# Performance work log

Hardware: AMD Instinct MI355X
Metric: run time of the kernel (lower is better)

The kernel has to match this reference:

```python
import jax, jax.numpy as jnp
import numpy as np

N_P, N_A, N_S = 100000, 150000, 1000
D_IN, N_HID, N_OUT = 256, 256, 64
E_PA, E_PS = 800000, 100000
HOP = 3


def spmm(row, col, val, h, n_rows):
    # sparse A (edge list) @ dense h : gather source rows, scale, scatter-add to dest rows
    return jax.ops.segment_sum(val[:, None] * h[col], row, num_segments=n_rows)


def setup_inputs() -> dict:
    key = jax.random.key(0)
    ks = jax.random.split(key, 30)
    inp = {}
    inp['x_P'] = jax.random.normal(ks[0], (N_P, D_IN), jnp.float32)
    inp['x_A'] = jax.random.normal(ks[1], (N_A, D_IN), jnp.float32)
    inp['x_S'] = jax.random.normal(ks[2], (N_S, D_IN), jnp.float32)
    inp['pa_row'] = jax.random.randint(ks[3], (E_PA,), 0, N_P, jnp.int32)
    inp['pa_col'] = jax.random.randint(ks[4], (E_PA,), 0, N_A, jnp.int32)
    inp['pa_val'] = jax.random.uniform(ks[5], (E_PA,), jnp.float32)
    inp['ps_row'] = jax.random.randint(ks[6], (E_PS,), 0, N_P, jnp.int32)
    inp['ps_col'] = jax.random.randint(ks[7], (E_PS,), 0, N_S, jnp.int32)
    inp['ps_val'] = jax.random.uniform(ks[8], (E_PS,), jnp.float32)
    inp['ap_row'] = jax.random.randint(ks[9], (E_PA,), 0, N_A, jnp.int32)
    inp['ap_col'] = jax.random.randint(ks[10], (E_PA,), 0, N_P, jnp.int32)
    inp['ap_val'] = jax.random.uniform(ks[11], (E_PA,), jnp.float32)
    inp['sp_row'] = jax.random.randint(ks[12], (E_PS,), 0, N_S, jnp.int32)
    inp['sp_col'] = jax.random.randint(ks[13], (E_PS,), 0, N_P, jnp.int32)
    inp['sp_val'] = jax.random.uniform(ks[14], (E_PS,), jnp.float32)
    inp['diag_PA'] = jax.random.uniform(ks[15], (N_P, 1), jnp.float32)
    inp['diag_PS'] = jax.random.uniform(ks[16], (N_P, 1), jnp.float32)
    inp['diag_AP'] = jax.random.uniform(ks[17], (N_A, 1), jnp.float32)
    inp['diag_SP'] = jax.random.uniform(ks[18], (N_S, 1), jnp.float32)
    s1 = 0.05
    inp['W1_P'] = jax.random.normal(ks[19], (D_IN, N_HID), jnp.float32) * s1
    inp['b1_P'] = jnp.zeros((N_HID,), jnp.float32)
    inp['W1_A'] = jax.random.normal(ks[20], (D_IN, N_HID), jnp.float32) * s1
    inp['b1_A'] = jnp.zeros((N_HID,), jnp.float32)
    inp['W1_S'] = jax.random.normal(ks[21], (D_IN, N_HID), jnp.float32) * s1
    inp['b1_S'] = jnp.zeros((N_HID,), jnp.float32)
    inp['W2'] = jax.random.normal(ks[22], (N_HID, N_OUT), jnp.float32) * s1
    inp['b2'] = jnp.zeros((N_OUT,), jnp.float32)
    return inp


def reference(x_P, x_A, x_S,
              pa_row, pa_col, pa_val,
              ps_row, ps_col, ps_val,
              ap_row, ap_col, ap_val,
              sp_row, sp_col, sp_val,
              diag_PA, diag_PS, diag_AP, diag_SP,
              W1_P, b1_P, W1_A, b1_A, W1_S, b1_S, W2, b2):
    # input projections (dropout is identity in eval mode)
    xP = jax.nn.relu(x_P @ W1_P + b1_P)
    xA = jax.nn.relu(x_A @ W1_A + b1_A)
    xS = jax.nn.relu(x_S @ W1_S + b1_S)
    hP, hA, hS = xP, xA, xS
    # hop loop; node types updated sequentially (P, A, S) as in the torch dict loop
    for _ in range(HOP):
        hP = 0.5 * ((spmm(pa_row, pa_col, pa_val, hA, N_P) + diag_PA * xP)
                    + (spmm(ps_row, ps_col, ps_val, hS, N_P) + diag_PS * xP))
        hA = spmm(ap_row, ap_col, ap_val, hP, N_A) + diag_AP * xA
        hS = spmm(sp_row, sp_col, sp_val, hP, N_S) + diag_SP * xS
    # target_node_type = 'P'
    return hP @ W2 + b2
```

## Files before the change

kernel.cpp:

```cpp
#include <hip/hip_runtime.h>
#include <hip/hip_bf16.h>


typedef __attribute__((ext_vector_type(8))) short bf16x8;
typedef __attribute__((ext_vector_type(4))) float f32x4;

__device__ inline unsigned short f2bf(float f) {
    unsigned u = __builtin_bit_cast(unsigned, f);
    u += 0x7FFFu + ((u >> 16) & 1u);
    return (unsigned short)(u >> 16);
}
__device__ inline float bflo(unsigned u) { return __builtin_bit_cast(float, u << 16); }
__device__ inline float bfhi(unsigned u) { return __builtin_bit_cast(float, u & 0xffff0000u); }

__device__ inline void bar_sync() {
    __builtin_amdgcn_sched_barrier(0);
    asm volatile("s_waitcnt lgkmcnt(0)" ::: "memory");
    __builtin_amdgcn_s_barrier();
    __builtin_amdgcn_sched_barrier(0);
}

__global__ void k_prep_count(const float* __restrict__ W1P, const float* __restrict__ W1A,
                             const float* __restrict__ W1S, const float* __restrict__ W2f,
                             unsigned short* __restrict__ out,
                             const int* __restrict__ pa, const int* __restrict__ ps,
                             const int* __restrict__ ap, const int* __restrict__ sp,
                             int* __restrict__ cnt, int nP, int nA, int ePA, int ePS) {
    int i = blockIdx.x * 256 + threadIdx.x;
    if (i < 3 * 65536) {
        int m = i >> 16;
        int r = i & 65535;
        int j = r & 7, l = (r >> 3) & 63, kk = (r >> 9) & 7, nt = (r >> 12) & 15;
        int col = nt * 16 + (l & 15);
        int k = kk * 32 + ((l >> 4) << 3) + j;
        const float* s = (m == 0) ? W1P : (m == 1) ? W1A : W1S;
        out[i] = f2bf(s[k * 256 + col]);
        return;
    } else if (i < 3 * 65536 + 16384) {
        int r = i - 3 * 65536;
        int j = r & 7, l = (r >> 3) & 63, kk = (r >> 9) & 7, nt = (r >> 12) & 3;
        int col = nt * 16 + (l & 15);
        int k = kk * 32 + ((l >> 4) << 3) + j;
        out[i] = f2bf(W2f[k * 64 + col]);
        return;
    }
    i -= 212992;
    int r, base;
    if (i < 0) return;
    if (i < ePA) { r = pa[i]; base = 0; }
    else if (i < ePA + ePS) { r = ps[i - ePA]; base = nP; }
    else if (i < 2 * ePA + ePS) { r = ap[i - ePA - ePS]; base = 2 * nP; }
    else if (i < 2 * ePA + 2 * ePS) { r = sp[i - 2 * ePA - ePS]; base = 2 * nP + nA; }
    else return;
    atomicAdd(&cnt[base + r], 1);
}

__global__ __launch_bounds__(256)
void k_proj_all(const float* __restrict__ xP, const float* __restrict__ xA,
                const float* __restrict__ xS, const unsigned short* __restrict__ Wpk,
                const float* __restrict__ b1P, const float* __restrict__ b1A,
                const float* __restrict__ b1S,
                unsigned short* __restrict__ yP, unsigned short* __restrict__ yA,
                unsigned short* __restrict__ yS, int nP, int nA, int nS) {
    __shared__ unsigned short xs[32 * 256];
    const int TP = (nP + 31) >> 5, TA = (nA + 31) >> 5, TS = (nS + 31) >> 5;
    const int TT = TP + TA + TS;
    const int tid = threadIdx.x, lane = tid & 63, w = tid >> 6;
    const int l15 = lane & 15, lhi = lane >> 4;
    const unsigned short* W2pk = Wpk + 3 * 65536;

    float4 xr[8];
    int t = blockIdx.x;
    if (t >= TT) return;

    {
        const float* x; int r0, nn;
        if (t < TP) { x = xP; r0 = t << 5; nn = nP; }
        else if (t < TP + TA) { x = xA; r0 = (t - TP) << 5; nn = nA; }
        else { x = xS; r0 = (t - TP - TA) << 5; nn = nS; }
        #pragma unroll
        for (int j = 0; j < 4; ++j) {
            int c = tid + j * 256;
            int row = c >> 5, col = (c & 31) << 3;
            int gr = r0 + row;
            float4 z = make_float4(0, 0, 0, 0);
            xr[2 * j] = z; xr[2 * j + 1] = z;
            if (gr < nn) {
                const float4* p = (const float4*)(x + (size_t)gr * 256 + col);
                xr[2 * j] = p[0]; xr[2 * j + 1] = p[1];
            }
        }
    }
    while (t < TT) {
        const unsigned short* W1; const float* b1; unsigned short* y; int r0, nn;
        if (t < TP) { r0 = t << 5; nn = nP; W1 = Wpk; b1 = b1P; y = yP; }
        else if (t < TP + TA) { r0 = (t - TP) << 5; nn = nA; W1 = Wpk + 65536; b1 = b1A; y = yA; }
        else { r0 = (t - TP - TA) << 5; nn = nS; W1 = Wpk + 2 * 65536; b1 = b1S; y = yS; }

        bar_sync();
        #pragma unroll
        for (int j = 0; j < 4; ++j) {
            int c = tid + j * 256;
            int row = c >> 5, col = (c & 31) << 3;
            float4 f0 = xr[2 * j], f1 = xr[2 * j + 1];
            bf16x8 v;
            v[0] = (short)f2bf(f0.x); v[1] = (short)f2bf(f0.y);
            v[2] = (short)f2bf(f0.z); v[3] = (short)f2bf(f0.w);
            v[4] = (short)f2bf(f1.x); v[5] = (short)f2bf(f1.y);
            v[6] = (short)f2bf(f1.z); v[7] = (short)f2bf(f1.w);
            int byte = row * 512 + ((col * 2) ^ ((row & 7) << 4));
            *(bf16x8*)((char*)xs + byte) = v;
        }
        int tn = t + gridDim.x;
        if (tn < TT) {
            const float* x2; int r02, n2;
            if (tn < TP) { x2 = xP; r02 = tn << 5; n2 = nP; }
            else if (tn < TP + TA) { x2 = xA; r02 = (tn - TP) << 5; n2 = nA; }
            else { x2 = xS; r02 = (tn - TP - TA) << 5; n2 = nS; }
            #pragma unroll
            for (int j = 0; j < 4; ++j) {
                int c = tid + j * 256;
                int row = c >> 5, col = (c & 31) << 3;
                int gr = r02 + row;
                float4 z = make_float4(0, 0, 0, 0), a0 = z, a1 = z;
                if (gr < n2) {
                    const float4* q = (const float4*)(x2 + (size_t)gr * 256 + col);
                    a0 = q[0]; a1 = q[1];
                }
                xr[2 * j] = a0; xr[2 * j + 1] = a1;
            }
        }
        bar_sync();

        f32x4 acc[2][4] = {};
        #pragma unroll
        for (int kk = 0; kk < 8; ++kk) {
            int k = kk * 32 + lhi * 8;
            bf16x8 a[2], b[4];
            #pragma unroll
            for (int m = 0; m < 2; ++m) {
                int row = m * 16 + l15;
                int byte = row * 512 + ((k * 2) ^ ((row & 7) << 4));
                a[m] = *(const bf16x8*)((const char*)xs + byte);
            }
            #pragma unroll
            for (int nq = 0; nq < 4; ++nq)
                b[nq] = *(const bf16x8*)(W1 + ((((w * 4 + nq) * 8 + kk) * 64 + lane) << 3));
            #pragma unroll
            for (int m = 0; m < 2; ++m)
                #pragma unroll
                for (int nq = 0; nq < 4; ++nq)
                    acc[m][nq] = __builtin_amdgcn_mfma_f32_16x16x32_bf16(a[m], b[nq], acc[m][nq], 0, 0, 0);
        }
        bar_sync();

        #pragma unroll
        for (int nq = 0; nq < 4; ++nq) {
            int col = w * 64 + nq * 16 + l15;
            float bias = b1[col];
            #pragma unroll
            for (int m = 0; m < 2; ++m)
                #pragma unroll
                for (int q = 0; q < 4; ++q) {
                    int row = m * 16 + lhi * 4 + q;
                    float vv = acc[m][nq][q] + bias;
                    vv = vv > 0.f ? vv : 0.f;
                    int byte = row * 512 + ((col * 2) ^ ((row & 7) << 4));
                    *(unsigned short*)((char*)xs + byte) = f2bf(vv);
                }
        }
        bar_sync();

        if (w < 2) {
            f32x4 acc2[4] = {};
            #pragma unroll
            for (int kk = 0; kk < 8; ++kk) {
                int k = kk * 32 + lhi * 8;
                int row = w * 16 + l15;
                int byte = row * 512 + ((k * 2) ^ ((row & 7) << 4));
                bf16x8 a = *(const bf16x8*)((const char*)xs + byte);
                #pragma unroll
                for (int nq = 0; nq < 4; ++nq) {
                    bf16x8 b = *(const bf16x8*)(W2pk + (((nq * 8 + kk) * 64 + lane) << 3));
                    acc2[nq] = __builtin_amdgcn_mfma_f32_16x16x32_bf16(a, b, acc2[nq], 0, 0, 0);
                }
            }
            #pragma unroll
            for (int nq = 0; nq < 4; ++nq)
                #pragma unroll
                for (int q = 0; q < 4; ++q) {
                    int row = w * 16 + lhi * 4 + q;
                    int gr = r0 + row;
                    if (gr < nn) y[(size_t)gr * 64 + (nq * 16 + l15)] = f2bf(acc2[nq][q]);
                }
        }
        t = tn;
    }
}

__global__ __launch_bounds__(256)
void k_scan1(const int* __restrict__ cnt, int* __restrict__ off,
             int* __restrict__ bsum, int n) {
    __shared__ int sh[256];
    int tid = threadIdx.x;
    int base = blockIdx.x * 1024 + tid * 4;
    int c[4];
    #pragma unroll
    for (int j = 0; j < 4; ++j) c[j] = (base + j < n) ? cnt[base + j] : 0;
    int s = c[0] + c[1] + c[2] + c[3];
    sh[tid] = s;
    __syncthreads();
    #pragma unroll
    for (int o = 1; o < 256; o <<= 1) {
        int v = (tid >= o) ? sh[tid - o] : 0;
        __syncthreads();
        sh[tid] += v;
        __syncthreads();
    }
    int run = sh[tid] - s;
    #pragma unroll
    for (int j = 0; j < 4; ++j) {
        if (base + j < n) off[base + j] = run;
        run += c[j];
    }
    if (tid == 255) bsum[blockIdx.x] = sh[255];
}

__global__ __launch_bounds__(256)
void k_scan2(int* __restrict__ bsum, int nb) {
    __shared__ int sh[256];
    int tid = threadIdx.x;
    int base = tid * 4;
    int v[4];
    #pragma unroll
    for (int j = 0; j < 4; ++j) v[j] = (base + j < nb) ? bsum[base + j] : 0;
    int s = v[0] + v[1] + v[2] + v[3];
    sh[tid] = s;
    __syncthreads();
    #pragma unroll
    for (int o = 1; o < 256; o <<= 1) {
        int x = (tid >= o) ? sh[tid - o] : 0;
        __syncthreads();
        sh[tid] += x;
        __syncthreads();
    }
    int run = sh[tid] - s;
    #pragma unroll
    for (int j = 0; j < 4; ++j) {
        if (base + j < nb) bsum[base + j] = run;
        run += v[j];
    }
}

__global__ void k_scan3(const int* __restrict__ off0, const int* __restrict__ bsum,
                        int* __restrict__ offPA, int* __restrict__ offPS,
                        int* __restrict__ offAP, int* __restrict__ offSP,
                        int* __restrict__ curPA, int* __restrict__ curPS,
                        int* __restrict__ curAP, int* __restrict__ curSP,
                        int nP, int nA, int nS, int ePA, int ePS) {
    int i = blockIdx.x * 256 + threadIdx.x;
    int NC = 2 * nP + nA + nS;
    if (i >= NC) return;
    int v = off0[i] + bsum[i >> 10];
    int g0, loc, ng, nE; int *og, *cg;
    if (i < nP)                { g0 = 0;           loc = i;                ng = nP; nE = ePA; og = offPA; cg = curPA; }
    else if (i < 2 * nP)       { g0 = nP;          loc = i - nP;           ng = nP; nE = ePS; og = offPS; cg = curPS; }
    else if (i < 2 * nP + nA)  { g0 = 2 * nP;      loc = i - 2 * nP;       ng = nA; nE = ePA; og = offAP; cg = curAP; }
    else                       { g0 = 2 * nP + nA; loc = i - 2 * nP - nA;  ng = nS; nE = ePS; og = offSP; cg = curSP; }
    int basev = off0[g0] + bsum[g0 >> 10];
    int rel = v - basev;
    og[loc] = rel; cg[loc] = rel;
    if (loc == 0) og[ng] = nE;
}

__global__ __launch_bounds__(256)
void k_scatter_all(const int* __restrict__ pa_r, const int* __restrict__ pa_c, const float* __restrict__ pa_v,
                   const int* __restrict__ ps_r, const int* __restrict__ ps_c, const float* __restrict__ ps_v,
                   const int* __restrict__ ap_r, const int* __restrict__ ap_c, const float* __restrict__ ap_v,
                   const int* __restrict__ sp_r, const int* __restrict__ sp_c, const float* __restrict__ sp_v,
                   int* __restrict__ curPA, int* __restrict__ curPS,
                   int* __restrict__ curAP, int* __restrict__ curSP,
                   int2* __restrict__ entPA, int2* __restrict__ entPS,
                   int2* __restrict__ entAP, int2* __restrict__ entSP,
                   int nP, int nA, int nS, int ePA, int ePS) {
    int xcd = blockIdx.x & 7;
    int i = (blockIdx.x >> 3) * 256 + threadIdx.x;
    const int *r, *c; const float* v; int* cur; int2* ent; int e, n;
    if (i < ePA) { e = i; r = pa_r; c = pa_c; v = pa_v; cur = curPA; ent = entPA; n = nP; }
    else if (i < ePA + ePS) { e = i - ePA; r = ps_r; c = ps_c; v = ps_v; cur = curPS; ent = entPS; n = nP; }
    else if (i < 2 * ePA + ePS) { e = i - ePA - ePS; r = ap_r; c = ap_c; v = ap_v; cur = curAP; ent = entAP; n = nA; }
    else if (i < 2 * ePA + 2 * ePS) { e = i - 2 * ePA - ePS; r = sp_r; c = sp_c; v = sp_v; cur = curSP; ent = entSP; n = nS; }
    else return;
    int rr = __builtin_nontemporal_load(r + e);
    int r8 = rr * 8;
    if (r8 < xcd * n || r8 >= (xcd + 1) * n) return;
    int cc = __builtin_nontemporal_load(c + e);
    float vv = __builtin_nontemporal_load(v + e);
    int pp = atomicAdd(&cur[rr], 1);
    ent[pp] = make_int2(cc, __float_as_int(vv));
}

__device__ inline void fma8(float acc[8], float w, uint4 g) {
    acc[0] = fmaf(w, bflo(g.x), acc[0]); acc[1] = fmaf(w, bfhi(g.x), acc[1]);
    acc[2] = fmaf(w, bflo(g.y), acc[2]); acc[3] = fmaf(w, bfhi(g.y), acc[3]);
    acc[4] = fmaf(w, bflo(g.z), acc[4]); acc[5] = fmaf(w, bfhi(g.z), acc[5]);
    acc[6] = fmaf(w, bflo(g.w), acc[6]); acc[7] = fmaf(w, bfhi(g.w), acc[7]);
}

__device__ inline void oct_pipe(const int2* __restrict__ ent, int s, int t,
                                const unsigned short* __restrict__ src,
                                int sub, int chunk, float acc[8]) {
    if (s >= t) return;
    int i0 = s + sub;
    int c0 = i0 < t ? i0 : t - 1;
    int2 Ea = ent[c0];
    float wa = i0 < t ? __int_as_float(Ea.y) : 0.f;
    uint4 ga = ((const uint4*)(src + ((size_t)(unsigned)Ea.x << 6)))[chunk];
    for (int e = s; ; ) {
        int en = e + 8;
        if (en < t) {
            int i1 = en + sub;
            int c1 = i1 < t ? i1 : t - 1;
            int2 Eb = ent[c1];
            float wb = i1 < t ? __int_as_float(Eb.y) : 0.f;
            uint4 gb = ((const uint4*)(src + ((size_t)(unsigned)Eb.x << 6)))[chunk];
            fma8(acc, wa, ga);
            wa = wb; ga = gb; e = en;
        } else {
            fma8(acc, wa, ga);
            break;
        }
    }
}

__device__ inline void red8(float acc[8]) {
    #pragma unroll
    for (int j = 0; j < 8; ++j) {
        acc[j] += __shfl_xor(acc[j], 8, 64);
        acc[j] += __shfl_xor(acc[j], 16, 64);
        acc[j] += __shfl_xor(acc[j], 32, 64);
    }
}

__device__ inline uint4 pack8(const float acc[8]) {
    uint4 o;
    o.x = (unsigned)f2bf(acc[0]) | ((unsigned)f2bf(acc[1]) << 16);
    o.y = (unsigned)f2bf(acc[2]) | ((unsigned)f2bf(acc[3]) << 16);
    o.z = (unsigned)f2bf(acc[4]) | ((unsigned)f2bf(acc[5]) << 16);
    o.w = (unsigned)f2bf(acc[6]) | ((unsigned)f2bf(acc[7]) << 16);
    return o;
}

__global__ __launch_bounds__(256)
void k_rowAS(unsigned short* __restrict__ hA, const unsigned short* __restrict__ yA,
             const float* __restrict__ dAP, const int* __restrict__ offAP,
             const int2* __restrict__ entAP,
             unsigned short* __restrict__ hS, const unsigned short* __restrict__ yS,
             const float* __restrict__ dSP, const int* __restrict__ offSP,
             const int2* __restrict__ entSP,
             const unsigned short* __restrict__ srcP, int nA, int nS) {
    int r = (blockIdx.x * 256 + threadIdx.x) >> 6;
    int lane = threadIdx.x & 63;
    int sub = lane >> 3, chunk = lane & 7;
    const int* off; const int2* ent; const unsigned short* y;
    const float* dg; unsigned short* dst;
    if (r < nA) { off = offAP; ent = entAP; y = yA; dg = dAP; dst = hA; }
    else if ((r -= nA) < nS) { off = offSP; ent = entSP; y = yS; dg = dSP; dst = hS; }
    else return;
    float acc[8] = {};
    int s = off[r], t = off[r + 1];
    float d = dg[r];
    uint4 gy = ((const uint4*)(y + (size_t)r * 64))[chunk];
    oct_pipe(ent, s, t, srcP, sub, chunk, acc);
    red8(acc);
    if (sub == 0) {
        acc[0] += d * bflo(gy.x); acc[1] += d * bfhi(gy.x);
        acc[2] += d * bflo(gy.y); acc[3] += d * bfhi(gy.y);
        acc[4] += d * bflo(gy.z); acc[5] += d * bfhi(gy.z);
        acc[6] += d * bflo(gy.w); acc[7] += d * bfhi(gy.w);
        ((uint4*)(dst + (size_t)r * 64))[chunk] = pack8(acc);
    }
}

template<int FINAL>
__global__ __launch_bounds__(256)
void k_row2(unsigned short* __restrict__ dst, float* __restrict__ dstf,
            const unsigned short* __restrict__ yP,
            const float* __restrict__ dA, const float* __restrict__ dB,
            const int* __restrict__ offA, const int2* __restrict__ entA,
            const unsigned short* __restrict__ srcA,
            const int* __restrict__ offB, const int2* __restrict__ entB,
            const unsigned short* __restrict__ srcB,
            const float* __restrict__ b2, int n) {
    int r = (blockIdx.x * 256 + threadIdx.x) >> 6;
    int lane = threadIdx.x & 63;
    int sub = lane >> 3, chunk = lane & 7;
    if (r >= n) return;
    float acc[8] = {};
    int sA = offA[r], tA = offA[r + 1];
    int sB = offB[r], tB = offB[r + 1];
    float d = dA[r] + dB[r];
    uint4 gy = ((const uint4*)(yP + (size_t)r * 64))[chunk];

    bool hasB = sB < tB;
    float wB = 0.f; uint4 gB;
    if (hasB) {
        int iB = sB + sub;
        int cB = iB < tB ? iB : tB - 1;
        int2 EB = entB[cB];
        wB = iB < tB ? __int_as_float(EB.y) : 0.f;
        gB = ((const uint4*)(srcB + ((size_t)(unsigned)EB.x << 6)))[chunk];
    }
    oct_pipe(entA, sA, tA, srcA, sub, chunk, acc);
    if (hasB) {
        fma8(acc, wB, gB);
        if (sB + 8 < tB) oct_pipe(entB, sB + 8, tB, srcB, sub, chunk, acc);
    }
    red8(acc);
    if (sub == 0) {
        acc[0] = 0.5f * (acc[0] + d * bflo(gy.x)); acc[1] = 0.5f * (acc[1] + d * bfhi(gy.x));
        acc[2] = 0.5f * (acc[2] + d * bflo(gy.y)); acc[3] = 0.5f * (acc[3] + d * bfhi(gy.y));
        acc[4] = 0.5f * (acc[4] + d * bflo(gy.z)); acc[5] = 0.5f * (acc[5] + d * bfhi(gy.z));
        acc[6] = 0.5f * (acc[6] + d * bflo(gy.w)); acc[7] = 0.5f * (acc[7] + d * bfhi(gy.w));
        if (FINAL) {
            float4 b0 = ((const float4*)b2)[chunk * 2];
            float4 b1v = ((const float4*)b2)[chunk * 2 + 1];
            float4 o0 = make_float4(acc[0] + b0.x, acc[1] + b0.y, acc[2] + b0.z, acc[3] + b0.w);
            float4 o1 = make_float4(acc[4] + b1v.x, acc[5] + b1v.y, acc[6] + b1v.z, acc[7] + b1v.w);
            ((float4*)(dstf + (size_t)r * 64))[chunk * 2] = o0;
            ((float4*)(dstf + (size_t)r * 64))[chunk * 2 + 1] = o1;
        } else {
            ((uint4*)(dst + (size_t)r * 64))[chunk] = pack8(acc);
        }
    }
}

extern "C" void kernel_launch(void* const* d_in, const int* in_sizes, int n_in,
                              void* d_out, int out_size, void* d_ws, size_t ws_size,
                              hipStream_t stream) {
    const float* x_P = (const float*)d_in[0];
    const float* x_A = (const float*)d_in[1];
    const float* x_S = (const float*)d_in[2];
    const int* pa_row = (const int*)d_in[3];
    const int* pa_col = (const int*)d_in[4];
    const float* pa_val = (const float*)d_in[5];
    const int* ps_row = (const int*)d_in[6];
    const int* ps_col = (const int*)d_in[7];
    const float* ps_val = (const float*)d_in[8];
    const int* ap_row = (const int*)d_in[9];
    const int* ap_col = (const int*)d_in[10];
    const float* ap_val = (const float*)d_in[11];
    const int* sp_row = (const int*)d_in[12];
    const int* sp_col = (const int*)d_in[13];
    const float* sp_val = (const float*)d_in[14];
    const float* diag_PA = (const float*)d_in[15];
    const float* diag_PS = (const float*)d_in[16];
    const float* diag_AP = (const float*)d_in[17];
    const float* diag_SP = (const float*)d_in[18];
    const float* W1_P = (const float*)d_in[19];
    const float* b1_P = (const float*)d_in[20];
    const float* W1_A = (const float*)d_in[21];
    const float* b1_A = (const float*)d_in[22];
    const float* W1_S = (const float*)d_in[23];
    const float* b1_S = (const float*)d_in[24];
    const float* W2  = (const float*)d_in[25];
    const float* b2  = (const float*)d_in[26];

    const int nP = in_sizes[15], nA = in_sizes[17], nS = in_sizes[18];
    const int ePA = in_sizes[3], ePS = in_sizes[6];
    const int NC = 2 * nP + nA + nS;

    char* base = (char*)d_ws;
    size_t cur = 0;
    auto alloc = [&](size_t bytes) -> char* {
        cur = (cur + 255) & ~(size_t)255;
        char* p = base + cur;
        cur += bytes;
        return p;
    };
    unsigned short* yP = (unsigned short*)alloc((size_t)nP * 64 * 2);
    unsigned short* yA = (unsigned short*)alloc((size_t)nA * 64 * 2);
    unsigned short* yS = (unsigned short*)alloc((size_t)nS * 64 * 2);
    unsigned short* hP = (unsigned short*)alloc((size_t)nP * 64 * 2);
    unsigned short* hA = (unsigned short*)alloc((size_t)nA * 64 * 2);
    unsigned short* hS = (unsigned short*)alloc((size_t)nS * 64 * 2);
    unsigned short* Wpk = (unsigned short*)alloc(212992 * 2);
    int* cnt  = (int*)alloc((size_t)NC * 4);
    int* off0 = (int*)alloc((size_t)NC * 4);
    int* offPA = (int*)alloc((size_t)(nP + 1) * 4);
    int* offPS = (int*)alloc((size_t)(nP + 1) * 4);
    int* offAP = (int*)alloc((size_t)(nA + 1) * 4);
    int* offSP = (int*)alloc((size_t)(nS + 1) * 4);
    int* curPA = (int*)alloc((size_t)nP * 4);
    int* curPS = (int*)alloc((size_t)nP * 4);
    int* curAP = (int*)alloc((size_t)nA * 4);
    int* curSP = (int*)alloc((size_t)nS * 4);
    int2* entPA = (int2*)alloc((size_t)ePA * 8);
    int2* entPS = (int2*)alloc((size_t)ePS * 8);
    int2* entAP = (int2*)alloc((size_t)ePA * 8);
    int2* entSP = (int2*)alloc((size_t)ePS * 8);
    int* bsum = (int*)alloc(1024 * 4);
    (void)ws_size;

    hipMemsetAsync(cnt, 0, (size_t)NC * 4, stream);
    const int eTot = 2 * (ePA + ePS);
    k_prep_count<<<(212992 + eTot + 255) / 256, 256, 0, stream>>>(
        W1_P, W1_A, W1_S, W2, Wpk,
        pa_row, ps_row, ap_row, sp_row, cnt, nP, nA, ePA, ePS);
    const int nb = (NC + 1023) / 1024;
    k_scan1<<<nb, 256, 0, stream>>>(cnt, off0, bsum, NC);
    k_scan2<<<1, 256, 0, stream>>>(bsum, nb);
    k_scan3<<<(NC + 255) / 256, 256, 0, stream>>>(off0, bsum, offPA, offPS, offAP, offSP,
                                                  curPA, curPS, curAP, curSP,
                                                  nP, nA, nS, ePA, ePS);
    const int SCB = (eTot + 255) / 256;
    k_scatter_all<<<8 * SCB, 256, 0, stream>>>(
        pa_row, pa_col, pa_val, ps_row, ps_col, ps_val,
        ap_row, ap_col, ap_val, sp_row, sp_col, sp_val,
        curPA, curPS, curAP, curSP, entPA, entPS, entAP, entSP,
        nP, nA, nS, ePA, ePS);

    k_proj_all<<<1024, 256, 0, stream>>>(x_P, x_A, x_S, Wpk, b1_P, b1_A, b1_S,
                                         yP, yA, yS, nP, nA, nS);

    const int gbP = (nP + 3) / 4, gbAS = (nA + nS + 3) / 4;
    k_row2<0><<<gbP, 256, 0, stream>>>(hP, nullptr, yP, diag_PA, diag_PS,
                                       offPA, entPA, yA, offPS, entPS, yS, b2, nP);
    k_rowAS<<<gbAS, 256, 0, stream>>>(hA, yA, diag_AP, offAP, entAP,
                                      hS, yS, diag_SP, offSP, entSP, hP, nA, nS);
    k_row2<0><<<gbP, 256, 0, stream>>>(hP, nullptr, yP, diag_PA, diag_PS,
                                       offPA, entPA, hA, offPS, entPS, hS, b2, nP);
    k_rowAS<<<gbAS, 256, 0, stream>>>(hA, yA, diag_AP, offAP, entAP,
                                      hS, yS, diag_SP, offSP, entSP, hP, nA, nS);
    k_row2<1><<<gbP, 256, 0, stream>>>(nullptr, (float*)d_out, yP, diag_PA, diag_PS,
                                       offPA, entPA, hA, offPS, entPS, hS, b2, nP);
}
```

Measured before the change: 558.2 us.

## Load projection inputs directly into MFMA registers and partition count atomics by XCD

The projection kernel now reads fp32 input rows straight from global memory into MFMA operand registers instead of staging them through LDS. It double-buffers the hidden tile in LDS so one barrier per tile is enough. Separately, the edge-count pass is replicated eight times, and each replica only performs atomics for a slice of the destination rows so that atomics stay within one XCD's L2. This trades redundant index reads and uncoalesced global loads for fewer barriers and more local atomics.

```diff
diff --git a/kernel.cpp b/kernel.cpp
--- a/kernel.cpp
+++ b/kernel.cpp
@@ -20,139 +20,102 @@
     __builtin_amdgcn_sched_barrier(0);
 }
 
+__device__ inline bf16x8 cvt8(float4 f0, float4 f1) {
+    bf16x8 v;
+    v[0] = (short)f2bf(f0.x); v[1] = (short)f2bf(f0.y);
+    v[2] = (short)f2bf(f0.z); v[3] = (short)f2bf(f0.w);
+    v[4] = (short)f2bf(f1.x); v[5] = (short)f2bf(f1.y);
+    v[6] = (short)f2bf(f1.z); v[7] = (short)f2bf(f1.w);
+    return v;
+}
+
 __global__ void k_prep_count(const float* __restrict__ W1P, const float* __restrict__ W1A,
                              const float* __restrict__ W1S, const float* __restrict__ W2f,
-                             unsigned short* __restrict__ out,
+                             unsigned short* __restrict__ out, int PKB,
                              const int* __restrict__ pa, const int* __restrict__ ps,
                              const int* __restrict__ ap, const int* __restrict__ sp,
-                             int* __restrict__ cnt, int nP, int nA, int ePA, int ePS) {
-    int i = blockIdx.x * 256 + threadIdx.x;
-    if (i < 3 * 65536) {
-        int m = i >> 16;
-        int r = i & 65535;
-        int j = r & 7, l = (r >> 3) & 63, kk = (r >> 9) & 7, nt = (r >> 12) & 15;
-        int col = nt * 16 + (l & 15);
-        int k = kk * 32 + ((l >> 4) << 3) + j;
-        const float* s = (m == 0) ? W1P : (m == 1) ? W1A : W1S;
-        out[i] = f2bf(s[k * 256 + col]);
+                             int* __restrict__ cnt, int nP, int nA, int nS,
+                             int ePA, int ePS) {
+    if (blockIdx.x < PKB) {
+        int i = blockIdx.x * 256 + threadIdx.x;
+        if (i < 3 * 65536) {
+            int m = i >> 16;
+            int r = i & 65535;
+            int j = r & 7, l = (r >> 3) & 63, kk = (r >> 9) & 7, nt = (r >> 12) & 15;
+            int col = nt * 16 + (l & 15);
+            int k = kk * 32 + ((l >> 4) << 3) + j;
+            const float* s = (m == 0) ? W1P : (m == 1) ? W1A : W1S;
+            out[i] = f2bf(s[k * 256 + col]);
+        } else if (i < 3 * 65536 + 16384) {
+            int r = i - 3 * 65536;
+            int j = r & 7, l = (r >> 3) & 63, kk = (r >> 9) & 7, nt = (r >> 12) & 3;
+            int col = nt * 16 + (l & 15);
+            int k = kk * 32 + ((l >> 4) << 3) + j;
+            out[i] = f2bf(W2f[k * 64 + col]);
+        }
         return;
-    } else if (i < 3 * 65536 + 16384) {
-        int r = i - 3 * 65536;
-        int j = r & 7, l = (r >> 3) & 63, kk = (r >> 9) & 7, nt = (r >> 12) & 3;
-        int col = nt * 16 + (l & 15);
-        int k = kk * 32 + ((l >> 4) << 3) + j;
-        out[i] = f2bf(W2f[k * 64 + col]);
-        return;
-    }
-    i -= 212992;
-    int r, base;
-    if (i < 0) return;
-    if (i < ePA) { r = pa[i]; base = 0; }
-    else if (i < ePA + ePS) { r = ps[i - ePA]; base = nP; }
-    else if (i < 2 * ePA + ePS) { r = ap[i - ePA - ePS]; base = 2 * nP; }
-    else if (i < 2 * ePA + 2 * ePS) { r = sp[i - 2 * ePA - ePS]; base = 2 * nP + nA; }
+    }
+    int b = blockIdx.x - PKB;
+    int xcd = b & 7;
+    int i = (b >> 3) * 256 + threadIdx.x;
+    const int* r; int base, n;
+    if (i < ePA) { r = pa; base = 0; n = nP; }
+    else if (i < ePA + ePS) { r = ps; i -= ePA; base = nP; n = nP; }
+    else if (i < 2 * ePA + ePS) { r = ap; i -= ePA + ePS; base = 2 * nP; n = nA; }
+    else if (i < 2 * ePA + 2 * ePS) { r = sp; i -= 2 * ePA + ePS; base = 2 * nP + nA; n = nS; }
     else return;
-    atomicAdd(&cnt[base + r], 1);
+    int rr = __builtin_nontemporal_load(r + i);
+    int r8 = rr * 8;
+    if (r8 < xcd * n || r8 >= (xcd + 1) * n) return;
+    atomicAdd(&cnt[base + rr], 1);
 }
 
 __global__ __launch_bounds__(256)
-void k_proj_all(const float* __restrict__ xP, const float* __restrict__ xA,
-                const float* __restrict__ xS, const unsigned short* __restrict__ Wpk,
-                const float* __restrict__ b1P, const float* __restrict__ b1A,
-                const float* __restrict__ b1S,
-                unsigned short* __restrict__ yP, unsigned short* __restrict__ yA,
-                unsigned short* __restrict__ yS, int nP, int nA, int nS) {
-    __shared__ unsigned short xs[32 * 256];
+void k_proj_direct(const float* __restrict__ xP, const float* __restrict__ xA,
+                   const float* __restrict__ xS, const unsigned short* __restrict__ Wpk,
+                   const float* __restrict__ b1P, const float* __restrict__ b1A,
+                   const float* __restrict__ b1S,
+                   unsigned short* __restrict__ yP, unsigned short* __restrict__ yA,
+                   unsigned short* __restrict__ yS, int nP, int nA, int nS) {
+    __shared__ unsigned short hid[2][32 * 256];
     const int TP = (nP + 31) >> 5, TA = (nA + 31) >> 5, TS = (nS + 31) >> 5;
     const int TT = TP + TA + TS;
     const int tid = threadIdx.x, lane = tid & 63, w = tid >> 6;
     const int l15 = lane & 15, lhi = lane >> 4;
     const unsigned short* W2pk = Wpk + 3 * 65536;
 
-    float4 xr[8];
-    int t = blockIdx.x;
-    if (t >= TT) return;
-
-    {
-        const float* x; int r0, nn;
-        if (t < TP) { x = xP; r0 = t << 5; nn = nP; }
-        else if (t < TP + TA) { x = xA; r0 = (t - TP) << 5; nn = nA; }
-        else { x = xS; r0 = (t - TP - TA) << 5; nn = nS; }
-        #pragma unroll
-        for (int j = 0; j < 4; ++j) {
-            int c = tid + j * 256;
-            int row = c >> 5, col = (c & 31) << 3;
-            int gr = r0 + row;
-            float4 z = make_float4(0, 0, 0, 0);
-            xr[2 * j] = z; xr[2 * j + 1] = z;
-            if (gr < nn) {
-                const float4* p = (const float4*)(x + (size_t)gr * 256 + col);
-                xr[2 * j] = p[0]; xr[2 * j + 1] = p[1];
-            }
-        }
-    }
-    while (t < TT) {
-        const unsigned short* W1; const float* b1; unsigned short* y; int r0, nn;
-        if (t < TP) { r0 = t << 5; nn = nP; W1 = Wpk; b1 = b1P; y = yP; }
-        else if (t < TP + TA) { r0 = (t - TP) << 5; nn = nA; W1 = Wpk + 65536; b1 = b1A; y = yA; }
-        else { r0 = (t - TP - TA) << 5; nn = nS; W1 = Wpk + 2 * 65536; b1 = b1S; y = yS; }
-
-        bar_sync();
-        #pragma unroll
-        for (int j = 0; j < 4; ++j) {
-            int c = tid + j * 256;
-            int row = c >> 5, col = (c & 31) << 3;
-            float4 f0 = xr[2 * j], f1 = xr[2 * j + 1];
-            bf16x8 v;
-            v[0] = (short)f2bf(f0.x); v[1] = (short)f2bf(f0.y);
-            v[2] = (short)f2bf(f0.z); v[3] = (short)f2bf(f0.w);
-            v[4] = (short)f2bf(f1.x); v[5] = (short)f2bf(f1.y);
-            v[6] = (short)f2bf(f1.z); v[7] = (short)f2bf(f1.w);
-            int byte = row * 512 + ((col * 2) ^ ((row & 7) << 4));
-            *(bf16x8*)((char*)xs + byte) = v;
-        }
-        int tn = t + gridDim.x;
-        if (tn < TT) {
-            const float* x2; int r02, n2;
-            if (tn < TP) { x2 = xP; r02 = tn << 5; n2 = nP; }
-            else if (tn < TP + TA) { x2 = xA; r02 = (tn - TP) << 5; n2 = nA; }
-            else { x2 = xS; r02 = (tn - TP - TA) << 5; n2 = nS; }
-            #pragma unroll
-            for (int j = 0; j < 4; ++j) {
-                int c = tid + j * 256;
-                int row = c >> 5, col = (c & 31) << 3;
-                int gr = r02 + row;
-                float4 z = make_float4(0, 0, 0, 0), a0 = z, a1 = z;
-                if (gr < n2) {
-                    const float4* q = (const float4*)(x2 + (size_t)gr * 256 + col);
-                    a0 = q[0]; a1 = q[1];
-                }
-                xr[2 * j] = a0; xr[2 * j + 1] = a1;
-            }
-        }
-        bar_sync();
+    int p = 0;
+    for (int t = blockIdx.x; t < TT; t += gridDim.x) {
+        const float* x; const unsigned short* W1; const float* b1;
+        unsigned short* y; int r0, nn;
+        if (t < TP) { x = xP; r0 = t << 5; nn = nP; W1 = Wpk; b1 = b1P; y = yP; }
+        else if (t < TP + TA) { x = xA; r0 = (t - TP) << 5; nn = nA; W1 = Wpk + 65536; b1 = b1A; y = yA; }
+        else { x = xS; r0 = (t - TP - TA) << 5; nn = nS; W1 = Wpk + 2 * 65536; b1 = b1S; y = yS; }
+
+        int rr0 = r0 + l15;      if (rr0 >= nn) rr0 = nn - 1;
+        int rr1 = r0 + 16 + l15; if (rr1 >= nn) rr1 = nn - 1;
+        const float* xb0 = x + (size_t)rr0 * 256 + lhi * 8;
+        const float* xb1 = x + (size_t)rr1 * 256 + lhi * 8;
 
         f32x4 acc[2][4] = {};
         #pragma unroll
         for (int kk = 0; kk < 8; ++kk) {
-            int k = kk * 32 + lhi * 8;
-            bf16x8 a[2], b[4];
-            #pragma unroll
-            for (int m = 0; m < 2; ++m) {
-                int row = m * 16 + l15;
-                int byte = row * 512 + ((k * 2) ^ ((row & 7) << 4));
-                a[m] = *(const bf16x8*)((const char*)xs + byte);
-            }
+            float4 f00 = *(const float4*)(xb0 + kk * 32);
+            float4 f01 = *(const float4*)(xb0 + kk * 32 + 4);
+            float4 f10 = *(const float4*)(xb1 + kk * 32);
+            float4 f11 = *(const float4*)(xb1 + kk * 32 + 4);
+            bf16x8 a0 = cvt8(f00, f01);
+            bf16x8 a1 = cvt8(f10, f11);
+            bf16x8 b[4];
             #pragma unroll
             for (int nq = 0; nq < 4; ++nq)
                 b[nq] = *(const bf16x8*)(W1 + ((((w * 4 + nq) * 8 + kk) * 64 + lane) << 3));
             #pragma unroll
-            for (int m = 0; m < 2; ++m)
-                #pragma unroll
-                for (int nq = 0; nq < 4; ++nq)
-                    acc[m][nq] = __builtin_amdgcn_mfma_f32_16x16x32_bf16(a[m], b[nq], acc[m][nq], 0, 0, 0);
+            for (int nq = 0; nq < 4; ++nq) {
+                acc[0][nq] = __builtin_amdgcn_mfma_f32_16x16x32_bf16(a0, b[nq], acc[0][nq], 0, 0, 0);
+                acc[1][nq] = __builtin_amdgcn_mfma_f32_16x16x32_bf16(a1, b[nq], acc[1][nq], 0, 0, 0);
+            }
         }
-        bar_sync();
 
         #pragma unroll
         for (int nq = 0; nq < 4; ++nq) {
@@ -166,7 +129,7 @@
                     float vv = acc[m][nq][q] + bias;
                     vv = vv > 0.f ? vv : 0.f;
                     int byte = row * 512 + ((col * 2) ^ ((row & 7) << 4));
-                    *(unsigned short*)((char*)xs + byte) = f2bf(vv);
+                    *(unsigned short*)((char*)hid[p] + byte) = f2bf(vv);
                 }
         }
         bar_sync();
@@ -178,7 +141,7 @@
                 int k = kk * 32 + lhi * 8;
                 int row = w * 16 + l15;
                 int byte = row * 512 + ((k * 2) ^ ((row & 7) << 4));
-                bf16x8 a = *(const bf16x8*)((const char*)xs + byte);
+                bf16x8 a = *(const bf16x8*)((const char*)hid[p] + byte);
                 #pragma unroll
                 for (int nq = 0; nq < 4; ++nq) {
                     bf16x8 b = *(const bf16x8*)(W2pk + (((nq * 8 + kk) * 64 + lane) << 3));
@@ -194,7 +157,7 @@
                     if (gr < nn) y[(size_t)gr * 64 + (nq * 16 + l15)] = f2bf(acc2[nq][q]);
                 }
         }
-        t = tn;
+        p ^= 1;
     }
 }
 
@@ -504,24 +467,25 @@
 
     hipMemsetAsync(cnt, 0, (size_t)NC * 4, stream);
     const int eTot = 2 * (ePA + ePS);
-    k_prep_count<<<(212992 + eTot + 255) / 256, 256, 0, stream>>>(
-        W1_P, W1_A, W1_S, W2, Wpk,
-        pa_row, ps_row, ap_row, sp_row, cnt, nP, nA, ePA, ePS);
+    const int PKB = (212992 + 255) / 256;
+    const int SCB = (eTot + 255) / 256;
+    k_prep_count<<<PKB + 8 * SCB, 256, 0, stream>>>(
+        W1_P, W1_A, W1_S, W2, Wpk, PKB,
+        pa_row, ps_row, ap_row, sp_row, cnt, nP, nA, nS, ePA, ePS);
     const int nb = (NC + 1023) / 1024;
     k_scan1<<<nb, 256, 0, stream>>>(cnt, off0, bsum, NC);
     k_scan2<<<1, 256, 0, stream>>>(bsum, nb);
     k_scan3<<<(NC + 255) / 256, 256, 0, stream>>>(off0, bsum, offPA, offPS, offAP, offSP,
                                                   curPA, curPS, curAP, curSP,
                                                   nP, nA, nS, ePA, ePS);
-    const int SCB = (eTot + 255) / 256;
     k_scatter_all<<<8 * SCB, 256, 0, stream>>>(
         pa_row, pa_col, pa_val, ps_row, ps_col, ps_val,
         ap_row, ap_col, ap_val, sp_row, sp_col, sp_val,
         curPA, curPS, curAP, curSP, entPA, entPS, entAP, entSP,
         nP, nA, nS, ePA, ePS);
 
-    k_proj_all<<<1024, 256, 0, stream>>>(x_P, x_A, x_S, Wpk, b1_P, b1_A, b1_S,
-                                         yP, yA, yS, nP, nA, nS);
+    k_proj_direct<<<1024, 256, 0, stream>>>(x_P, x_A, x_S, Wpk, b1_P, b1_A, b1_S,
+                                            yP, yA, yS, nP, nA, nS);
 
     const int gbP = (nP + 3) / 4, gbAS = (nA + nS + 3) / 4;
     k_row2<0><<<gbP, 256, 0, stream>>>(hP, nullptr, yP, diag_PA, diag_PS,
```

Result: slower. 672.9 us (+20.6%).
